# Performance work log

Hardware: AMD Instinct MI355X
Metric: run time of the kernel (lower is better)

Reference implementation:

```python
import jax, jax.numpy as jnp
import numpy as np

NUM_HEADS = 8
# iRPE 'product' piecewise params with ratio=1.9
ALPHA, BETA, GAMMA = 1.9, 3.8, 15.2
BETA_INT = 4                       # round(BETA)
S = 2 * BETA_INT + 1               # 9 buckets per axis
NUM_BUCKETS = S * S                # 81


def _piecewise_index(d):
    # d: float relative coordinate; linear inside |d|<=alpha, log-spaced outside, clipped at beta
    ad = jnp.abs(d)
    log_part = jnp.sign(d) * jnp.round(
        jnp.minimum(ALPHA + jnp.log(jnp.maximum(ad, ALPHA) / ALPHA)
                    / np.log(GAMMA / ALPHA) * (BETA - ALPHA), BETA))
    idx = jnp.where(ad <= ALPHA, jnp.round(d), log_part)
    return jnp.clip(idx, -BETA_INT, BETA_INT).astype(jnp.int32)


def _bucket_ids(side):
    # 2D product bucketing over a side x side grid -> [N, N] int32 bucket ids in [0, 81)
    coords = jnp.stack(jnp.meshgrid(jnp.arange(side), jnp.arange(side), indexing='ij'),
                       axis=-1).reshape(-1, 2).astype(jnp.float32)
    diff = coords[:, None, :] - coords[None, :, :]          # [N, N, 2]
    by = _piecewise_index(diff[..., 0]) + BETA_INT
    bx = _piecewise_index(diff[..., 1]) + BETA_INT
    return by * S + bx


def _layernorm(x, g, b):
    mu = jnp.mean(x, axis=-1, keepdims=True)
    var = jnp.mean(jnp.square(x - mu), axis=-1, keepdims=True)
    return (x - mu) * jax.lax.rsqrt(var + 1e-5) * g + b


def _mlp(x, w1, b1, w2, b2):
    h = jax.nn.gelu(x @ w1 + b1, approximate=False)
    return h @ w2 + b2


def _attention(q, k, v, bucket, tq, tk, tv, wp, bp):
    # q,k,v: [B, N, C]; bucket: [N, N]; tq/tk/tv: [81, hd] (shared across heads)
    B, Nq, C = q.shape
    Nk = k.shape[1]
    hd = C // NUM_HEADS
    scale = hd ** -0.5
    qh = q.reshape(B, Nq, NUM_HEADS, hd).transpose(0, 2, 1, 3)   # [B,H,Nq,hd]
    kh = k.reshape(B, Nk, NUM_HEADS, hd).transpose(0, 2, 1, 3)
    vh = v.reshape(B, Nk, NUM_HEADS, hd).transpose(0, 2, 1, 3)
    attn = jnp.einsum('bhid,bhjd->bhij', qh, kh) * scale          # [B,H,Nq,Nk]
    # rpe_k: contextual bias from q: q . tk[bucket(i,j)]
    lk = jnp.einsum('bhid,cd->bhic', qh, tk)                      # [B,H,Nq,81]
    rows = jnp.arange(Nq)[:, None]
    attn = attn + lk[:, :, rows, bucket]
    # rpe_q: contextual bias from scaled k, then transposed onto (i,j)
    lq = jnp.einsum('bhjd,cd->bhjc', kh * scale, tq)              # [B,H,Nk,81]
    bq = lq[:, :, jnp.arange(Nk)[:, None], bucket]                # [B,H,Nk,Nq] (j,i)
    attn = attn + bq.transpose(0, 1, 3, 2)
    attn = jax.nn.softmax(attn, axis=-1)
    outh = jnp.einsum('bhij,bhjd->bhid', attn, vh)
    # rpe_v: attn-weighted sum of tv[bucket(i,j)]
    outh = outh + jnp.einsum('bhij,ijd->bhid', attn, tv[bucket])
    out = outh.transpose(0, 2, 1, 3).reshape(B, Nq, C)
    return out @ wp + bp


def setup_inputs() -> dict:
    key = jax.random.key(0)
    ks = jax.random.split(key, 16)
    B, N, C, H = 4, 1024, 512, 2048
    w = lambda k, s: (jax.random.normal(k, s, jnp.float32) * 0.02)
    return {
        'x0': jax.random.normal(ks[0], (B, N, C), jnp.float32),
        'x1': jax.random.normal(ks[1], (B, N, C), jnp.float32),
        'ln00_g': jnp.ones((C,), jnp.float32), 'ln00_b': jnp.zeros((C,), jnp.float32),
        'ln01_g': jnp.ones((C,), jnp.float32), 'ln01_b': jnp.zeros((C,), jnp.float32),
        'ln10_g': jnp.ones((C,), jnp.float32), 'ln10_b': jnp.zeros((C,), jnp.float32),
        'ln11_g': jnp.ones((C,), jnp.float32), 'ln11_b': jnp.zeros((C,), jnp.float32),
        'w_qkv0': w(ks[2], (C, 3 * C)), 'b_qkv0': jnp.zeros((3 * C,), jnp.float32),
        'w_qkv1': w(ks[3], (C, 3 * C)), 'b_qkv1': jnp.zeros((3 * C,), jnp.float32),
        'w_proj': w(ks[4], (C, C)), 'b_proj': jnp.zeros((C,), jnp.float32),
        'table_q': w(ks[5], (NUM_BUCKETS, C // NUM_HEADS)),
        'table_k': w(ks[6], (NUM_BUCKETS, C // NUM_HEADS)),
        'table_v': w(ks[7], (NUM_BUCKETS, C // NUM_HEADS)),
        'w_fc1_0': w(ks[8], (C, H)), 'b_fc1_0': jnp.zeros((H,), jnp.float32),
        'w_fc2_0': w(ks[9], (H, C)), 'b_fc2_0': jnp.zeros((C,), jnp.float32),
        'w_fc1_1': w(ks[10], (C, H)), 'b_fc1_1': jnp.zeros((H,), jnp.float32),
        'w_fc2_1': w(ks[11], (H, C)), 'b_fc2_1': jnp.zeros((C,), jnp.float32),
    }


def reference(x0, x1, ln00_g, ln00_b, ln01_g, ln01_b, ln10_g, ln10_b, ln11_g, ln11_b,
              w_qkv0, b_qkv0, w_qkv1, b_qkv1, w_proj, b_proj,
              table_q, table_k, table_v,
              w_fc1_0, b_fc1_0, w_fc2_0, b_fc2_0, w_fc1_1, b_fc1_1, w_fc2_1, b_fc2_1):
    B, N, C = x0.shape
    side = int(np.sqrt(N))
    bucket = _bucket_ids(side)                                   # [N, N]
    qkv0 = _layernorm(x0, ln00_g, ln00_b) @ w_qkv0 + b_qkv0
    q0, k0, v0 = jnp.split(qkv0, 3, axis=-1)
    qkv1 = _layernorm(x1, ln01_g, ln01_b) @ w_qkv1 + b_qkv1
    q1, k1, v1 = jnp.split(qkv1, 3, axis=-1)
    # shared cross-attention module (same proj + rpe tables both directions)
    x0 = x0 + _attention(q0, k1, v1, bucket, table_q, table_k, table_v, w_proj, b_proj)
    x1 = x1 + _attention(q1, k0, v0, bucket, table_q, table_k, table_v, w_proj, b_proj)
    x0 = x0 + _mlp(_layernorm(x0, ln10_g, ln10_b), w_fc1_0, b_fc1_0, w_fc2_0, b_fc2_0)
    x1 = x1 + _mlp(_layernorm(x1, ln11_g, ln11_b), w_fc1_1, b_fc1_1, w_fc2_1, b_fc2_1)
    return (x0, x1)
```

## Files before the change

kernel.cpp:

```cpp
#include <hip/hip_runtime.h>
#include <hip/hip_bf16.h>
#include <math.h>

#define NFULL 1024
#define CDIM  512
#define HD    64
#define NH    8

typedef __attribute__((ext_vector_type(8))) short s16x8;
typedef __attribute__((ext_vector_type(4))) short s16x4;
typedef __attribute__((ext_vector_type(4))) float f32x4;

__device__ __forceinline__ float b2f(unsigned short u) {
  return __uint_as_float((unsigned)u << 16);
}
__device__ __forceinline__ unsigned short f2b(float f) {
  unsigned u = __float_as_uint(f);
  return (unsigned short)((u + 0x7FFFu + ((u >> 16) & 1u)) >> 16);
}

__device__ __forceinline__ int pwidx(int d) {
  int ad = d < 0 ? -d : d;
  if (ad <= 1) return d;
  float v = 1.9f + logf((float)ad * (1.0f / 1.9f)) * (1.9f / 2.0794415416798357f);
  v = fminf(v, 3.8f);
  int m = (int)rintf(v);
  if (m > 4) m = 4;
  return d > 0 ? m : -m;
}

__global__ __launch_bounds__(256) void ln_kernel(const float* __restrict__ x,
                                                 const float* __restrict__ g,
                                                 const float* __restrict__ be,
                                                 __hip_bfloat16* __restrict__ y) {
  __shared__ float red[8];
  int row = blockIdx.x, tid = threadIdx.x;
  const float* xr = x + (size_t)row * CDIM;
  float v0 = xr[tid], v1 = xr[tid + 256];
  float s = v0 + v1;
#pragma unroll
  for (int off = 32; off; off >>= 1) s += __shfl_xor(s, off);
  int wid = tid >> 6, lane = tid & 63;
  if (!lane) red[wid] = s;
  __syncthreads();
  float mu = (red[0] + red[1] + red[2] + red[3]) * (1.0f / 512.0f);
  float d0 = v0 - mu, d1 = v1 - mu;
  float q = d0 * d0 + d1 * d1;
#pragma unroll
  for (int off = 32; off; off >>= 1) q += __shfl_xor(q, off);
  if (!lane) red[4 + wid] = q;
  __syncthreads();
  float var = (red[4] + red[5] + red[6] + red[7]) * (1.0f / 512.0f);
  float rstd = rsqrtf(var + 1e-5f);
  __hip_bfloat16* yr = y + (size_t)row * CDIM;
  yr[tid]       = __float2bfloat16(d0 * rstd * g[tid]       + be[tid]);
  yr[tid + 256] = __float2bfloat16(d1 * rstd * g[tid + 256] + be[tid + 256]);
}

__global__ __launch_bounds__(256) void wtrans_kernel(const float* __restrict__ W,
                                                     __hip_bfloat16* __restrict__ Wt,
                                                     int K, int N) {
  __shared__ float t[32][33];
  int n0 = blockIdx.x * 32, k0 = blockIdx.y * 32;
  int c = threadIdx.x, r0 = threadIdx.y;
#pragma unroll
  for (int rr = 0; rr < 32; rr += 8) t[r0 + rr][c] = W[(size_t)(k0 + r0 + rr) * N + n0 + c];
  __syncthreads();
#pragma unroll
  for (int rr = 0; rr < 32; rr += 8)
    Wt[(size_t)(n0 + r0 + rr) * K + k0 + c] = __float2bfloat16(t[c][r0 + rr]);
}

__device__ __forceinline__ float gelu_f(float x) {
  return 0.5f * x * (1.0f + erff(x * 0.7071067811865475f));
}

template <int ACT, int RES, int OUTBF>
__global__ __launch_bounds__(256, 1) void gemm_bf16(const short* __restrict__ A,
                                                    const short* __restrict__ Bt,
                                                    const float* __restrict__ bias,
                                                    const float* __restrict__ res,
                                                    void* __restrict__ Cout,
                                                    int M, int N, int K) {
  __shared__ __attribute__((aligned(16))) short As[128 * 40];
  __shared__ __attribute__((aligned(16))) short Bs[128 * 40];
  const int tid = threadIdx.x;
  const int bm = blockIdx.y * 128, bn = blockIdx.x * 128;
  const int w = tid >> 6, l = tid & 63;
  const int wr = w >> 1, wc = w & 1;
  const int lr = l & 15, lg = l >> 4;
  const int sr = tid >> 1, sh = (tid & 1) * 16;

  f32x4 acc[4][4] = {};

  for (int k0 = 0; k0 < K; k0 += 32) {
    __syncthreads();
    const float4* ga = (const float4*)(A + (size_t)(bm + sr) * K + k0 + sh);
    const float4* gb = (const float4*)(Bt + (size_t)(bn + sr) * K + k0 + sh);
    float4 a0 = ga[0], a1 = ga[1];
    float4 b0 = gb[0], b1 = gb[1];
    *(float4*)&As[sr * 40 + sh]     = a0;
    *(float4*)&As[sr * 40 + sh + 8] = a1;
    *(float4*)&Bs[sr * 40 + sh]     = b0;
    *(float4*)&Bs[sr * 40 + sh + 8] = b1;
    __syncthreads();
    s16x8 af[4], bf[4];
#pragma unroll
    for (int mi = 0; mi < 4; ++mi)
      af[mi] = *(const s16x8*)&As[(wr * 64 + mi * 16 + lr) * 40 + lg * 8];
#pragma unroll
    for (int ni = 0; ni < 4; ++ni)
      bf[ni] = *(const s16x8*)&Bs[(wc * 64 + ni * 16 + lr) * 40 + lg * 8];
#pragma unroll
    for (int mi = 0; mi < 4; ++mi)
#pragma unroll
      for (int ni = 0; ni < 4; ++ni)
        acc[mi][ni] = __builtin_amdgcn_mfma_f32_16x16x32_bf16(af[mi], bf[ni], acc[mi][ni], 0, 0, 0);
  }
  float bv[4];
#pragma unroll
  for (int ni = 0; ni < 4; ++ni) bv[ni] = bias[bn + wc * 64 + ni * 16 + lr];
#pragma unroll
  for (int mi = 0; mi < 4; ++mi) {
#pragma unroll
    for (int j = 0; j < 4; ++j) {
      int row = bm + wr * 64 + mi * 16 + lg * 4 + j;
#pragma unroll
      for (int ni = 0; ni < 4; ++ni) {
        int col = bn + wc * 64 + ni * 16 + lr;
        float vv = acc[mi][ni][j] + bv[ni];
        if (ACT) vv = gelu_f(vv);
        if (RES) vv += res[(size_t)row * N + col];
        if (OUTBF) ((__hip_bfloat16*)Cout)[(size_t)row * N + col] = __float2bfloat16(vv);
        else       ((float*)Cout)[(size_t)row * N + col] = vv;
      }
    }
  }
}

__global__ __launch_bounds__(256) void prep_kernel(const short* __restrict__ qkvb,
                                                   short* __restrict__ Qb,
                                                   short* __restrict__ Kb,
                                                   short* __restrict__ Vtb) {
  __shared__ short vlds[64 * 72];
  const int tid = threadIdx.x;
  const int n0 = blockIdx.x * 64;
  const int b = blockIdx.y;

#pragma unroll 4
  for (int it = 0; it < 32; ++it) {
    int e = tid + it * 256;
    int n = e >> 7, c8 = (e & 127) * 8;
    s16x8 v = *(const s16x8*)(qkvb + ((size_t)(b * NFULL + n0 + n)) * 1536 + c8);
    int hh = c8 >> 6, d8 = c8 & 63;
    if (hh < 8)
      *(s16x8*)(Qb + ((size_t)(b * 8 + hh) * NFULL + n0 + n) * 64 + d8) = v;
    else
      *(s16x8*)(Kb + ((size_t)(b * 8 + hh - 8) * NFULL + n0 + n) * 64 + d8) = v;
  }
  for (int hh = 0; hh < 8; ++hh) {
    __syncthreads();
#pragma unroll
    for (int rep = 0; rep < 2; ++rep) {
      int n = (tid >> 3) + rep * 32, d8 = (tid & 7) * 8;
      *(s16x8*)&vlds[n * 72 + d8] =
          *(const s16x8*)(qkvb + ((size_t)(b * NFULL + n0 + n)) * 1536 + 1024 + hh * 64 + d8);
    }
    __syncthreads();
#pragma unroll
    for (int rep = 0; rep < 2; ++rep) {
      int d = (tid >> 3) + rep * 32, n8 = (tid & 7) * 8;
      s16x8 o;
#pragma unroll
      for (int u = 0; u < 8; ++u) o[u] = vlds[(n8 + u) * 72 + d];
      *(s16x8*)(Vtb + ((size_t)(b * 8 + hh) * 64 + d) * NFULL + n0 + n8) = o;
    }
  }
}

__global__ __launch_bounds__(256) void bias_gemm(const short* __restrict__ Xb,
                                                 const float* __restrict__ Tg,
                                                 short* __restrict__ outg,
                                                 float scl) {
  __shared__ __attribute__((aligned(16))) short tlds[96 * 88];
  const int tid = threadIdx.x;
  const int w = tid >> 6, l = tid & 63;
  const int g = l >> 4, i15 = l & 15;
  const int tile = blockIdx.x, h = blockIdx.y, b = blockIdx.z;
  const size_t bh = (size_t)(b * NH + h);

  for (int f = tid; f < 81 * 16; f += 256) {
    int c = f >> 4, d4 = (f & 15) * 4;
    float4 t4 = *(const float4*)&Tg[c * 64 + d4];
    s16x4 s4 = {(short)f2b(t4.x), (short)f2b(t4.y), (short)f2b(t4.z), (short)f2b(t4.w)};
    *(s16x4*)&tlds[c * 88 + d4] = s4;
  }
  __syncthreads();

  const int r0w = tile * 128 + w * 32;
  s16x8 af[2][2];
#pragma unroll
  for (int nk = 0; nk < 2; ++nk) {
    const short* xr = Xb + (bh * NFULL + r0w + nk * 16 + i15) * 64 + g * 8;
    af[nk][0] = *(const s16x8*)(xr);
    af[nk][1] = *(const s16x8*)(xr + 32);
  }
#pragma unroll
  for (int c0i = 0; c0i < 6; ++c0i) {
    int c0 = c0i * 16;
    s16x8 bf0 = *(const s16x8*)&tlds[(c0 + i15) * 88 + g * 8];
    s16x8 bf1 = *(const s16x8*)&tlds[(c0 + i15) * 88 + 32 + g * 8];
#pragma unroll
    for (int nk = 0; nk < 2; ++nk) {
      f32x4 acc = {0.f, 0.f, 0.f, 0.f};
      acc = __builtin_amdgcn_mfma_f32_16x16x32_bf16(af[nk][0], bf0, acc, 0, 0, 0);
      acc = __builtin_amdgcn_mfma_f32_16x16x32_bf16(af[nk][1], bf1, acc, 0, 0, 0);
      int c = c0 + i15;
      if (c < 81) {
#pragma unroll
        for (int r = 0; r < 4; ++r) {
          int n = r0w + nk * 16 + g * 4 + r;
          outg[(bh * NFULL + n) * 84 + c] = (short)f2b(acc[r] * scl);
        }
      }
    }
  }
}

__global__ __launch_bounds__(256, 3) void attn_mfma(const short* __restrict__ Qb,
                                                    const short* __restrict__ Kb,
                                                    const short* __restrict__ Vtb,
                                                    const short* __restrict__ lkg,
                                                    const short* __restrict__ lqg,
                                                    const float* __restrict__ tv,
                                                    __hip_bfloat16* __restrict__ o) {
  __shared__ __attribute__((aligned(16))) short pbuf[4][1024];
  __shared__ float wbf[64 * 81];
  __shared__ __attribute__((aligned(16))) float tvf[81 * 64];
  __shared__ short pwy9[63], pwx4[63];

  const int tid = threadIdx.x;
  const int w = tid >> 6, l = tid & 63;
  const int g = l >> 4, i15 = l & 15;
  const int i0 = blockIdx.x * 64;
  const int h = blockIdx.y, b = blockIdx.z;
  const size_t bh = (size_t)(b * NH + h);
  const int i = i0 + w * 16 + i15;

  for (int f = tid; f < 1296; f += 256) ((float4*)tvf)[f] = ((const float4*)tv)[f];
  for (int f = tid; f < 5184; f += 256) wbf[f] = 0.f;
  if (tid < 63) {
    int pv = pwidx(tid - 31);
    pwy9[tid] = (short)((pv + 4) * 9);
    pwx4[tid] = (short)(pv + 4);
  }
  __syncthreads();

  const short* qrow = Qb + (bh * NFULL + i) * 64 + g * 8;
  const s16x8 qf0 = *(const s16x8*)(qrow);
  const s16x8 qf1 = *(const s16x8*)(qrow + 32);
  const unsigned short* lkrow = (const unsigned short*)(lkg + (bh * NFULL + i) * 84);
  const unsigned short* lqb = (const unsigned short*)(lqg + bh * NFULL * 84);
  const short* Kbase = Kb + bh * NFULL * 64;
  const short* Vbase = Vtb + bh * 64 * NFULL;
  const int iy = i >> 5, ix = i & 31;
  char* pwc = (char*)&pbuf[w][0];
  const int swz = (i15 & 7) << 4;
  float* wrow = &wbf[(w * 16 + i15) * 81];

  f32x4 oacc[4] = {};
  float psum = 0.f;

  for (int T = 0; T < 16; ++T) {
    const int j0 = T * 64;
    s16x8 kf[4][2], vf[4][2];
#pragma unroll
    for (int jc = 0; jc < 4; ++jc) {
      const short* kr = Kbase + (size_t)(j0 + jc * 16 + i15) * 64 + g * 8;
      kf[jc][0] = *(const s16x8*)(kr);
      kf[jc][1] = *(const s16x8*)(kr + 32);
    }
#pragma unroll
    for (int nc = 0; nc < 4; ++nc) {
      const short* vr = Vbase + (size_t)(nc * 16 + i15) * NFULL + j0 + g * 8;
      vf[nc][0] = *(const s16x8*)(vr);
      vf[nc][1] = *(const s16x8*)(vr + 32);
    }
    f32x4 sacc[4];
    const f32x4 zz = {0.f, 0.f, 0.f, 0.f};
#pragma unroll
    for (int jc = 0; jc < 4; ++jc) {
      sacc[jc] = __builtin_amdgcn_mfma_f32_16x16x32_bf16(kf[jc][0], qf0, zz, 0, 0, 0);
      sacc[jc] = __builtin_amdgcn_mfma_f32_16x16x32_bf16(kf[jc][1], qf1, sacc[jc], 0, 0, 0);
    }
#pragma unroll
    for (int jc = 0; jc < 4; ++jc) {
      s16x4 pv4;
#pragma unroll
      for (int r = 0; r < 4; ++r) {
        int j = j0 + jc * 16 + g * 4 + r;
        int jy = j >> 5, jx = j & 31;
        int bb = (int)pwy9[iy - jy + 31] + (int)pwx4[ix - jx + 31];
        float sv = sacc[jc][r] * 0.125f + b2f(lkrow[bb]) + b2f(lqb[(size_t)j * 84 + 80 - bb]);
        float p = __expf(sv);
        psum += p;
        atomicAdd(&wrow[bb], p);
        pv4[r] = (short)f2b(p);
      }
      *(s16x4*)(pwc + i15 * 128 + ((jc * 32 + g * 8) ^ swz)) = pv4;
    }
    s16x8 pbf0 = *(const s16x8*)(pwc + i15 * 128 + ((16 * g) ^ swz));
    s16x8 pbf1 = *(const s16x8*)(pwc + i15 * 128 + ((64 + 16 * g) ^ swz));
#pragma unroll
    for (int nc = 0; nc < 4; ++nc) {
      oacc[nc] = __builtin_amdgcn_mfma_f32_16x16x32_bf16(vf[nc][0], pbf0, oacc[nc], 0, 0, 0);
      oacc[nc] = __builtin_amdgcn_mfma_f32_16x16x32_bf16(vf[nc][1], pbf1, oacc[nc], 0, 0, 0);
    }
  }

  psum += __shfl_xor(psum, 16);
  psum += __shfl_xor(psum, 32);
  const float rn = 1.0f / psum;

  float tva[4][4] = {};
  for (int c1 = 0; c1 < 81; ++c1) {
    float wv = wrow[c1];
#pragma unroll
    for (int nc = 0; nc < 4; ++nc) {
      float4 t4 = *(const float4*)&tvf[c1 * 64 + nc * 16 + g * 4];
      tva[nc][0] = fmaf(wv, t4.x, tva[nc][0]);
      tva[nc][1] = fmaf(wv, t4.y, tva[nc][1]);
      tva[nc][2] = fmaf(wv, t4.z, tva[nc][2]);
      tva[nc][3] = fmaf(wv, t4.w, tva[nc][3]);
    }
  }

  short* ob = (short*)o + ((size_t)b * NFULL + i) * CDIM + h * 64;
#pragma unroll
  for (int nc = 0; nc < 4; ++nc) {
    s16x4 o4;
#pragma unroll
    for (int r = 0; r < 4; ++r) o4[r] = (short)f2b((oacc[nc][r] + tva[nc][r]) * rn);
    *(s16x4*)(ob + nc * 16 + g * 4) = o4;
  }
}

extern "C" void kernel_launch(void* const* d_in, const int* in_sizes, int n_in,
                              void* d_out, int out_size, void* d_ws, size_t ws_size,
                              hipStream_t stream) {
  (void)in_sizes; (void)n_in; (void)out_size; (void)ws_size;
  const float* x0 = (const float*)d_in[0];
  const float* x1 = (const float*)d_in[1];
  const float* ln00_g = (const float*)d_in[2];
  const float* ln00_b = (const float*)d_in[3];
  const float* ln01_g = (const float*)d_in[4];
  const float* ln01_b = (const float*)d_in[5];
  const float* ln10_g = (const float*)d_in[6];
  const float* ln10_b = (const float*)d_in[7];
  const float* ln11_g = (const float*)d_in[8];
  const float* ln11_b = (const float*)d_in[9];
  const float* w_qkv0 = (const float*)d_in[10];
  const float* b_qkv0 = (const float*)d_in[11];
  const float* w_qkv1 = (const float*)d_in[12];
  const float* b_qkv1 = (const float*)d_in[13];
  const float* w_proj = (const float*)d_in[14];
  const float* b_proj = (const float*)d_in[15];
  const float* table_q = (const float*)d_in[16];
  const float* table_k = (const float*)d_in[17];
  const float* table_v = (const float*)d_in[18];
  const float* w_fc1_0 = (const float*)d_in[19];
  const float* b_fc1_0 = (const float*)d_in[20];
  const float* w_fc2_0 = (const float*)d_in[21];
  const float* b_fc2_0 = (const float*)d_in[22];
  const float* w_fc1_1 = (const float*)d_in[23];
  const float* b_fc1_1 = (const float*)d_in[24];
  const float* w_fc2_1 = (const float*)d_in[25];
  const float* b_fc2_1 = (const float*)d_in[26];

  char* base = (char*)d_ws;
  short* qkvb0 = (short*)(base + 0);
  short* qkvb1 = (short*)(base + 12582912);
  short* Qb0   = (short*)(base + 25165824);
  short* Kb0   = (short*)(base + 29360128);
  short* Vtb0  = (short*)(base + 33554432);
  short* Qb1   = (short*)(base + 37748736);
  short* Kb1   = (short*)(base + 41943040);
  short* Vtb1  = (short*)(base + 46137344);
  short* lkg   = (short*)(base + 50331648);
  short* lqg   = (short*)(base + 55836672);
  short* obuf  = (short*)(base + 61341696);
  __hip_bfloat16* xnb = (__hip_bfloat16*)(base + 65536000);
  __hip_bfloat16* wq0t  = (__hip_bfloat16*)(base + 69730304);
  __hip_bfloat16* wq1t  = (__hip_bfloat16*)(base + 71303168);
  __hip_bfloat16* wpt   = (__hip_bfloat16*)(base + 72876032);
  __hip_bfloat16* wf10t = (__hip_bfloat16*)(base + 73400320);
  __hip_bfloat16* wf20t = (__hip_bfloat16*)(base + 75497472);
  __hip_bfloat16* wf11t = (__hip_bfloat16*)(base + 77594624);
  __hip_bfloat16* wf21t = (__hip_bfloat16*)(base + 79691776);
  short* hbufb = (short*)(base + 0);
  float* dout0 = (float*)d_out;
  float* dout1 = dout0 + (size_t)4 * 1024 * 512;

  const int M = 4096;

  wtrans_kernel<<<dim3(48, 16), dim3(32, 8), 0, stream>>>(w_qkv0, wq0t, 512, 1536);
  wtrans_kernel<<<dim3(48, 16), dim3(32, 8), 0, stream>>>(w_qkv1, wq1t, 512, 1536);
  wtrans_kernel<<<dim3(16, 16), dim3(32, 8), 0, stream>>>(w_proj, wpt, 512, 512);
  wtrans_kernel<<<dim3(64, 16), dim3(32, 8), 0, stream>>>(w_fc1_0, wf10t, 512, 2048);
  wtrans_kernel<<<dim3(16, 64), dim3(32, 8), 0, stream>>>(w_fc2_0, wf20t, 2048, 512);
  wtrans_kernel<<<dim3(64, 16), dim3(32, 8), 0, stream>>>(w_fc1_1, wf11t, 512, 2048);
  wtrans_kernel<<<dim3(16, 64), dim3(32, 8), 0, stream>>>(w_fc2_1, wf21t, 2048, 512);

  ln_kernel<<<M, 256, 0, stream>>>(x0, ln00_g, ln00_b, xnb);
  gemm_bf16<0, 0, 1><<<dim3(12, 32), 256, 0, stream>>>((const short*)xnb, (const short*)wq0t,
                                                       b_qkv0, nullptr, qkvb0, M, 1536, 512);
  ln_kernel<<<M, 256, 0, stream>>>(x1, ln01_g, ln01_b, xnb);
  gemm_bf16<0, 0, 1><<<dim3(12, 32), 256, 0, stream>>>((const short*)xnb, (const short*)wq1t,
                                                       b_qkv1, nullptr, qkvb1, M, 1536, 512);

  prep_kernel<<<dim3(16, 4), 256, 0, stream>>>(qkvb0, Qb0, Kb0, Vtb0);
  prep_kernel<<<dim3(16, 4), 256, 0, stream>>>(qkvb1, Qb1, Kb1, Vtb1);

  bias_gemm<<<dim3(8, 8, 4), 256, 0, stream>>>(Qb0, table_k, lkg, 1.0f);
  bias_gemm<<<dim3(8, 8, 4), 256, 0, stream>>>(Kb1, table_q, lqg, 0.125f);
  attn_mfma<<<dim3(16, 8, 4), 256, 0, stream>>>(Qb0, Kb1, Vtb1, lkg, lqg, table_v,
                                                (__hip_bfloat16*)obuf);
  gemm_bf16<0, 1, 0><<<dim3(4, 32), 256, 0, stream>>>(obuf, (const short*)wpt,
                                                      b_proj, x0, dout0, M, 512, 512);

  bias_gemm<<<dim3(8, 8, 4), 256, 0, stream>>>(Qb1, table_k, lkg, 1.0f);
  bias_gemm<<<dim3(8, 8, 4), 256, 0, stream>>>(Kb0, table_q, lqg, 0.125f);
  attn_mfma<<<dim3(16, 8, 4), 256, 0, stream>>>(Qb1, Kb0, Vtb0, lkg, lqg, table_v,
                                                (__hip_bfloat16*)obuf);
  gemm_bf16<0, 1, 0><<<dim3(4, 32), 256, 0, stream>>>(obuf, (const short*)wpt,
                                                      b_proj, x1, dout1, M, 512, 512);

  ln_kernel<<<M, 256, 0, stream>>>(dout0, ln10_g, ln10_b, xnb);
  gemm_bf16<1, 0, 1><<<dim3(16, 32), 256, 0, stream>>>((const short*)xnb, (const short*)wf10t,
                                                       b_fc1_0, nullptr, hbufb, M, 2048, 512);
  gemm_bf16<0, 1, 0><<<dim3(4, 32), 256, 0, stream>>>(hbufb, (const short*)wf20t,
                                                      b_fc2_0, dout0, dout0, M, 512, 2048);

  ln_kernel<<<M, 256, 0, stream>>>(dout1, ln11_g, ln11_b, xnb);
  gemm_bf16<1, 0, 1><<<dim3(16, 32), 256, 0, stream>>>((const short*)xnb, (const short*)wf11t,
                                                       b_fc1_1, nullptr, hbufb, M, 2048, 512);
  gemm_bf16<0, 1, 0><<<dim3(4, 32), 256, 0, stream>>>(hbufb, (const short*)wf21t,
                                                      b_fc2_1, dout1, dout1, M, 512, 2048);
}
```

Before: 864.5 us.

## Double-buffer K/V register loads and stage lk rows in LDS in attention kernel

```diff
diff --git a/kernel.cpp b/kernel.cpp
--- a/kernel.cpp
+++ b/kernel.cpp
@@ -227,6 +227,72 @@
   }
 }
 
+#define ATTN_STEP(J0, J0N, KF, VF, KFN, VFN, BY0, BY1, BY0N, BY1N)                       \
+  {                                                                                      \
+                              \
+    unsigned short lqv[4][4];                                                            \
+    _Pragma("unroll") for (int jc = 0; jc < 4; ++jc) {                                   \
+      _Pragma("unroll") for (int r = 0; r < 4; ++r) {                                    \
+        int bb = ((jc & 2) ? (BY1) : (BY0)) + bx8[jc & 1][r];                            \
+        lqv[jc][r] = lqb[(size_t)((J0) + jc * 16 + g * 4 + r) * 84 + 80 - bb];           \
+      }                                                                                  \
+    }                                                                                    \
+                                                    \
+    f32x4 sacc[4];                                                                       \
+    _Pragma("unroll") for (int jc = 0; jc < 4; ++jc) {                                   \
+      f32x4 zz = {0.f, 0.f, 0.f, 0.f};                                                   \
+      sacc[jc] = __builtin_amdgcn_mfma_f32_16x16x32_bf16(KF[jc][0], qf0, zz, 0, 0, 0);   \
+      sacc[jc] = __builtin_amdgcn_mfma_f32_16x16x32_bf16(KF[jc][1], qf1, sacc[jc], 0, 0, 0); \
+    }                                                                                    \
+                          \
+    {                                                                                    \
+      int j0w = (J0N) & 1023;                                                            \
+      _Pragma("unroll") for (int jc = 0; jc < 4; ++jc) {                                 \
+        const short* kr = Kb_h + (size_t)(j0w + jc * 16 + i15) * 64 + g * 8;             \
+        KFN[jc][0] = *(const s16x8*)(kr);                                                \
+        KFN[jc][1] = *(const s16x8*)(kr + 32);                                           \
+      }                                                                                  \
+      _Pragma("unroll") for (int nc = 0; nc < 4; ++nc) {                                 \
+        const short* vr = Vb_h + (size_t)(nc * 16 + i15) * NFULL + j0w + g * 8;          \
+        VFN[nc][0] = *(const s16x8*)(vr);                                                \
+        VFN[nc][1] = *(const s16x8*)(vr + 32);                                           \
+      }                                                                                  \
+      int jy0n = j0w >> 5;                                                               \
+      BY0N = (int)pwy9s[iy - jy0n + 31];                                                 \
+      BY1N = (int)pwy9s[iy - jy0n + 30];                                                 \
+    }                                                                                    \
+                                                             \
+    s16x4 pvall[4];                                                                      \
+    _Pragma("unroll") for (int jc = 0; jc < 4; ++jc) {                                   \
+      s16x4 pv4;                                                                         \
+      _Pragma("unroll") for (int r = 0; r < 4; ++r) {                                    \
+        int bb = ((jc & 2) ? (BY1) : (BY0)) + bx8[jc & 1][r];                            \
+        float sv = sacc[jc][r] * 0.125f + b2f(lkw[bb]) + b2f(lqv[jc][r]);                \
+        float p = __expf(sv);                                                            \
+        psum += p;                                                                       \
+        pv4[r] = (short)f2b(p);                                                          \
+      }                                                                                  \
+      pvall[jc] = pv4;                                                                   \
+      *(s16x4*)(pwc + i15 * 128 + ((jc * 32 + g * 8) ^ swz)) = pv4;                      \
+    }                                                                                    \
+                                                                         \
+    {                                                                                    \
+      s16x8 pbf0 = *(const s16x8*)(pwc + i15 * 128 + ((16 * g) ^ swz));                  \
+      s16x8 pbf1 = *(const s16x8*)(pwc + i15 * 128 + ((64 + 16 * g) ^ swz));             \
+      _Pragma("unroll") for (int nc = 0; nc < 4; ++nc) {                                 \
+        oacc[nc] = __builtin_amdgcn_mfma_f32_16x16x32_bf16(VF[nc][0], pbf0, oacc[nc], 0, 0, 0); \
+        oacc[nc] = __builtin_amdgcn_mfma_f32_16x16x32_bf16(VF[nc][1], pbf1, oacc[nc], 0, 0, 0); \
+      }                                                                                  \
+    }                                                                                    \
+                           \
+    _Pragma("unroll") for (int jc = 0; jc < 4; ++jc) {                                   \
+      _Pragma("unroll") for (int r = 0; r < 4; ++r) {                                    \
+        int bb = ((jc & 2) ? (BY1) : (BY0)) + bx8[jc & 1][r];                            \
+        atomicAdd(&wbf[rowi * 81 + bb], b2f((unsigned short)pvall[jc][r]));              \
+      }                                                                                  \
+    }                                                                                    \
+  }
+
 __global__ __launch_bounds__(256, 3) void attn_mfma(const short* __restrict__ Qb,
                                                     const short* __restrict__ Kb,
                                                     const short* __restrict__ Vtb,
@@ -234,88 +300,75 @@
                                                     const short* __restrict__ lqg,
                                                     const float* __restrict__ tv,
                                                     __hip_bfloat16* __restrict__ o) {
+  __shared__ __attribute__((aligned(16))) short lkb[64 * 84];
   __shared__ __attribute__((aligned(16))) short pbuf[4][1024];
   __shared__ float wbf[64 * 81];
-  __shared__ __attribute__((aligned(16))) float tvf[81 * 64];
-  __shared__ short pwy9[63], pwx4[63];
+  __shared__ short pwy9s[64], pwx4s[64];
 
   const int tid = threadIdx.x;
   const int w = tid >> 6, l = tid & 63;
   const int g = l >> 4, i15 = l & 15;
-  const int i0 = blockIdx.x * 64;
-  const int h = blockIdx.y, b = blockIdx.z;
+  const int f = blockIdx.x + 16 * (blockIdx.y + 8 * blockIdx.z);
+  const int hb = f & 31, tile = f >> 5;
+  const int b = hb >> 3, h = hb & 7;
+  const int i0 = tile * 64;
   const size_t bh = (size_t)(b * NH + h);
   const int i = i0 + w * 16 + i15;
-
-  for (int f = tid; f < 1296; f += 256) ((float4*)tvf)[f] = ((const float4*)tv)[f];
-  for (int f = tid; f < 5184; f += 256) wbf[f] = 0.f;
-  if (tid < 63) {
-    int pv = pwidx(tid - 31);
-    pwy9[tid] = (short)((pv + 4) * 9);
-    pwx4[tid] = (short)(pv + 4);
+  const int rowi = w * 16 + i15;
+
+  {
+    const s16x4* lksrc = (const s16x4*)(lkg + (bh * NFULL + i0) * 84);
+    for (int ff = tid; ff < 1344; ff += 256) ((s16x4*)lkb)[ff] = lksrc[ff];
+    for (int ff = tid; ff < 5184; ff += 256) wbf[ff] = 0.f;
+    if (tid < 63) {
+      int pv = pwidx(tid - 31);
+      pwy9s[tid] = (short)((pv + 4) * 9);
+      pwx4s[tid] = (short)(pv + 4);
+    }
   }
   __syncthreads();
 
   const short* qrow = Qb + (bh * NFULL + i) * 64 + g * 8;
   const s16x8 qf0 = *(const s16x8*)(qrow);
   const s16x8 qf1 = *(const s16x8*)(qrow + 32);
-  const unsigned short* lkrow = (const unsigned short*)(lkg + (bh * NFULL + i) * 84);
+  const short* Kb_h = Kb + bh * NFULL * 64;
+  const short* Vb_h = Vtb + bh * 64 * NFULL;
   const unsigned short* lqb = (const unsigned short*)(lqg + bh * NFULL * 84);
-  const short* Kbase = Kb + bh * NFULL * 64;
-  const short* Vbase = Vtb + bh * 64 * NFULL;
+  const unsigned short* lkw = (const unsigned short*)lkb + rowi * 84;
   const int iy = i >> 5, ix = i & 31;
   char* pwc = (char*)&pbuf[w][0];
   const int swz = (i15 & 7) << 4;
-  float* wrow = &wbf[(w * 16 + i15) * 81];
+
+  int bx8[2][4];
+#pragma unroll
+  for (int hi = 0; hi < 2; ++hi)
+#pragma unroll
+    for (int r = 0; r < 4; ++r) bx8[hi][r] = (int)pwx4s[ix - (hi * 16 + g * 4 + r) + 31];
 
   f32x4 oacc[4] = {};
   float psum = 0.f;
 
-  for (int T = 0; T < 16; ++T) {
-    const int j0 = T * 64;
-    s16x8 kf[4][2], vf[4][2];
-#pragma unroll
-    for (int jc = 0; jc < 4; ++jc) {
-      const short* kr = Kbase + (size_t)(j0 + jc * 16 + i15) * 64 + g * 8;
-      kf[jc][0] = *(const s16x8*)(kr);
-      kf[jc][1] = *(const s16x8*)(kr + 32);
-    }
-#pragma unroll
-    for (int nc = 0; nc < 4; ++nc) {
-      const short* vr = Vbase + (size_t)(nc * 16 + i15) * NFULL + j0 + g * 8;
-      vf[nc][0] = *(const s16x8*)(vr);
-      vf[nc][1] = *(const s16x8*)(vr + 32);
-    }
-    f32x4 sacc[4];
-    const f32x4 zz = {0.f, 0.f, 0.f, 0.f};
-#pragma unroll
-    for (int jc = 0; jc < 4; ++jc) {
-      sacc[jc] = __builtin_amdgcn_mfma_f32_16x16x32_bf16(kf[jc][0], qf0, zz, 0, 0, 0);
-      sacc[jc] = __builtin_amdgcn_mfma_f32_16x16x32_bf16(kf[jc][1], qf1, sacc[jc], 0, 0, 0);
-    }
-#pragma unroll
-    for (int jc = 0; jc < 4; ++jc) {
-      s16x4 pv4;
-#pragma unroll
-      for (int r = 0; r < 4; ++r) {
-        int j = j0 + jc * 16 + g * 4 + r;
-        int jy = j >> 5, jx = j & 31;
-        int bb = (int)pwy9[iy - jy + 31] + (int)pwx4[ix - jx + 31];
-        float sv = sacc[jc][r] * 0.125f + b2f(lkrow[bb]) + b2f(lqb[(size_t)j * 84 + 80 - bb]);
-        float p = __expf(sv);
-        psum += p;
-        atomicAdd(&wrow[bb], p);
-        pv4[r] = (short)f2b(p);
-      }
-      *(s16x4*)(pwc + i15 * 128 + ((jc * 32 + g * 8) ^ swz)) = pv4;
-    }
-    s16x8 pbf0 = *(const s16x8*)(pwc + i15 * 128 + ((16 * g) ^ swz));
-    s16x8 pbf1 = *(const s16x8*)(pwc + i15 * 128 + ((64 + 16 * g) ^ swz));
-#pragma unroll
-    for (int nc = 0; nc < 4; ++nc) {
-      oacc[nc] = __builtin_amdgcn_mfma_f32_16x16x32_bf16(vf[nc][0], pbf0, oacc[nc], 0, 0, 0);
-      oacc[nc] = __builtin_amdgcn_mfma_f32_16x16x32_bf16(vf[nc][1], pbf1, oacc[nc], 0, 0, 0);
-    }
+  s16x8 kfA[4][2], vfA[4][2], kfB[4][2], vfB[4][2];
+  int by0A, by1A, by0B, by1B;
+#pragma unroll
+  for (int jc = 0; jc < 4; ++jc) {
+    const short* kr = Kb_h + (size_t)(jc * 16 + i15) * 64 + g * 8;
+    kfA[jc][0] = *(const s16x8*)(kr);
+    kfA[jc][1] = *(const s16x8*)(kr + 32);
+  }
+#pragma unroll
+  for (int nc = 0; nc < 4; ++nc) {
+    const short* vr = Vb_h + (size_t)(nc * 16 + i15) * NFULL + g * 8;
+    vfA[nc][0] = *(const s16x8*)(vr);
+    vfA[nc][1] = *(const s16x8*)(vr + 32);
+  }
+  by0A = (int)pwy9s[iy + 31];
+  by1A = (int)pwy9s[iy + 30];
+
+  for (int t2 = 0; t2 < 8; ++t2) {
+    const int j0 = t2 * 128;
+    ATTN_STEP(j0, j0 + 64, kfA, vfA, kfB, vfB, by0A, by1A, by0B, by1B)
+    ATTN_STEP(j0 + 64, j0 + 128, kfB, vfB, kfA, vfA, by0B, by1B, by0A, by1A)
   }
 
   psum += __shfl_xor(psum, 16);
@@ -324,10 +377,10 @@
 
   float tva[4][4] = {};
   for (int c1 = 0; c1 < 81; ++c1) {
-    float wv = wrow[c1];
+    float wv = wbf[rowi * 81 + c1];
 #pragma unroll
     for (int nc = 0; nc < 4; ++nc) {
-      float4 t4 = *(const float4*)&tvf[c1 * 64 + nc * 16 + g * 4];
+      float4 t4 = *(const float4*)(tv + c1 * 64 + nc * 16 + g * 4);
       tva[nc][0] = fmaf(wv, t4.x, tva[nc][0]);
       tva[nc][1] = fmaf(wv, t4.y, tva[nc][1]);
       tva[nc][2] = fmaf(wv, t4.z, tva[nc][2]);
```

Result: slower. 895.4 us (+3.6%).

## Split attention keys across waves with 16-query tiles and LDS reduction

Applied to the files above, without the earlier changes.

```diff
diff --git a/kernel.cpp b/kernel.cpp
--- a/kernel.cpp
+++ b/kernel.cpp
@@ -227,121 +227,183 @@
   }
 }
 
-__global__ __launch_bounds__(256, 3) void attn_mfma(const short* __restrict__ Qb,
+__global__ __launch_bounds__(256, 2) void attn_mfma(const short* __restrict__ Qb,
                                                     const short* __restrict__ Kb,
                                                     const short* __restrict__ Vtb,
                                                     const short* __restrict__ lkg,
                                                     const short* __restrict__ lqg,
                                                     const float* __restrict__ tv,
                                                     __hip_bfloat16* __restrict__ o) {
+  __shared__ __attribute__((aligned(16))) short lkb[16 * 84];
   __shared__ __attribute__((aligned(16))) short pbuf[4][1024];
-  __shared__ float wbf[64 * 81];
-  __shared__ __attribute__((aligned(16))) float tvf[81 * 64];
-  __shared__ short pwy9[63], pwx4[63];
+  __shared__ float wbf[4][16 * 81];
+  __shared__ float obuf[1024];
+  __shared__ float psums[4][16];
+  __shared__ short pwy9s[64], pwx4s[64];
 
   const int tid = threadIdx.x;
   const int w = tid >> 6, l = tid & 63;
   const int g = l >> 4, i15 = l & 15;
-  const int i0 = blockIdx.x * 64;
-  const int h = blockIdx.y, b = blockIdx.z;
+  const int f = blockIdx.x + 64 * blockIdx.y + 512 * blockIdx.z;
+  const int h = f & 7, tile = (f >> 3) & 63, b = f >> 9;
+  const int i0 = tile * 16;
   const size_t bh = (size_t)(b * NH + h);
-  const int i = i0 + w * 16 + i15;
-
-  for (int f = tid; f < 1296; f += 256) ((float4*)tvf)[f] = ((const float4*)tv)[f];
-  for (int f = tid; f < 5184; f += 256) wbf[f] = 0.f;
-  if (tid < 63) {
-    int pv = pwidx(tid - 31);
-    pwy9[tid] = (short)((pv + 4) * 9);
-    pwx4[tid] = (short)(pv + 4);
+  const int i = i0 + i15;
+
+  {
+    const s16x4* lksrc = (const s16x4*)(lkg + (bh * NFULL + i0) * 84);
+    for (int ff = tid; ff < 336; ff += 256) ((s16x4*)lkb)[ff] = lksrc[ff];
+    float* wflat = &wbf[0][0];
+    for (int ff = tid; ff < 5184; ff += 256) wflat[ff] = 0.f;
+    for (int ff = tid; ff < 1024; ff += 256) obuf[ff] = 0.f;
+    if (tid < 63) {
+      int pv = pwidx(tid - 31);
+      pwy9s[tid] = (short)((pv + 4) * 9);
+      pwx4s[tid] = (short)(pv + 4);
+    }
   }
   __syncthreads();
 
   const short* qrow = Qb + (bh * NFULL + i) * 64 + g * 8;
   const s16x8 qf0 = *(const s16x8*)(qrow);
   const s16x8 qf1 = *(const s16x8*)(qrow + 32);
-  const unsigned short* lkrow = (const unsigned short*)(lkg + (bh * NFULL + i) * 84);
+  const short* Kb_h = Kb + bh * NFULL * 64;
+  const short* Vb_h = Vtb + bh * 64 * NFULL;
   const unsigned short* lqb = (const unsigned short*)(lqg + bh * NFULL * 84);
-  const short* Kbase = Kb + bh * NFULL * 64;
-  const short* Vbase = Vtb + bh * 64 * NFULL;
+  const unsigned short* lkw = (const unsigned short*)lkb + i15 * 84;
   const int iy = i >> 5, ix = i & 31;
   char* pwc = (char*)&pbuf[w][0];
   const int swz = (i15 & 7) << 4;
-  float* wrow = &wbf[(w * 16 + i15) * 81];
+  float* wrow = &wbf[w][i15 * 81];
+
+  int bx8[2][4];
+#pragma unroll
+  for (int hi = 0; hi < 2; ++hi)
+#pragma unroll
+    for (int r = 0; r < 4; ++r) bx8[hi][r] = (int)pwx4s[ix - (hi * 16 + g * 4 + r) + 31];
 
   f32x4 oacc[4] = {};
   float psum = 0.f;
 
-  for (int T = 0; T < 16; ++T) {
-    const int j0 = T * 64;
-    s16x8 kf[4][2], vf[4][2];
+#pragma unroll
+  for (int T = 0; T < 4; ++T) {
+    const int j0 = w * 256 + T * 64;
+    const int jy0 = (j0 >> 5);
+    const int by0 = (int)pwy9s[iy - jy0 + 31];
+    const int by1 = (int)pwy9s[iy - jy0 + 30];
+
+    s16x8 kf[4][2];
 #pragma unroll
     for (int jc = 0; jc < 4; ++jc) {
-      const short* kr = Kbase + (size_t)(j0 + jc * 16 + i15) * 64 + g * 8;
+      const short* kr = Kb_h + (size_t)(j0 + jc * 16 + i15) * 64 + g * 8;
       kf[jc][0] = *(const s16x8*)(kr);
       kf[jc][1] = *(const s16x8*)(kr + 32);
     }
+    unsigned short lqv[4][4];
+#pragma unroll
+    for (int jc = 0; jc < 4; ++jc)
+#pragma unroll
+      for (int r = 0; r < 4; ++r) {
+        int bb = ((jc & 2) ? by1 : by0) + bx8[jc & 1][r];
+        lqv[jc][r] = lqb[(size_t)(j0 + jc * 16 + g * 4 + r) * 84 + 80 - bb];
+      }
+    f32x4 sacc[4];
+#pragma unroll
+    for (int jc = 0; jc < 4; ++jc) {
+      f32x4 zz = {0.f, 0.f, 0.f, 0.f};
+      sacc[jc] = __builtin_amdgcn_mfma_f32_16x16x32_bf16(kf[jc][0], qf0, zz, 0, 0, 0);
+      sacc[jc] = __builtin_amdgcn_mfma_f32_16x16x32_bf16(kf[jc][1], qf1, sacc[jc], 0, 0, 0);
+    }
+    s16x4 pvall[4];
+#pragma unroll
+    for (int jc = 0; jc < 4; ++jc) {
+      s16x4 pv4;
+#pragma unroll
+      for (int r = 0; r < 4; ++r) {
+        int bb = ((jc & 2) ? by1 : by0) + bx8[jc & 1][r];
+        float sv = sacc[jc][r] * 0.125f + b2f(lkw[bb]) + b2f(lqv[jc][r]);
+        float p = __expf(sv);
+        psum += p;
+        pv4[r] = (short)f2b(p);
+      }
+      pvall[jc] = pv4;
+      *(s16x4*)(pwc + i15 * 128 + ((jc * 32 + g * 8) ^ swz)) = pv4;
+    }
+    s16x8 vf[4][2];
 #pragma unroll
     for (int nc = 0; nc < 4; ++nc) {
-      const short* vr = Vbase + (size_t)(nc * 16 + i15) * NFULL + j0 + g * 8;
+      const short* vr = Vb_h + (size_t)(nc * 16 + i15) * NFULL + j0 + g * 8;
       vf[nc][0] = *(const s16x8*)(vr);
       vf[nc][1] = *(const s16x8*)(vr + 32);
     }
-    f32x4 sacc[4];
-    const f32x4 zz = {0.f, 0.f, 0.f, 0.f};
-#pragma unroll
-    for (int jc = 0; jc < 4; ++jc) {
-      sacc[jc] = __builtin_amdgcn_mfma_f32_16x16x32_bf16(kf[jc][0], qf0, zz, 0, 0, 0);
-      sacc[jc] = __builtin_amdgcn_mfma_f32_16x16x32_bf16(kf[jc][1], qf1, sacc[jc], 0, 0, 0);
-    }
-#pragma unroll
-    for (int jc = 0; jc < 4; ++jc) {
-      s16x4 pv4;
+    {
+      s16x8 pbf0 = *(const s16x8*)(pwc + i15 * 128 + ((16 * g) ^ swz));
+      s16x8 pbf1 = *(const s16x8*)(pwc + i15 * 128 + ((64 + 16 * g) ^ swz));
+#pragma unroll
+      for (int nc = 0; nc < 4; ++nc) {
+        oacc[nc] = __builtin_amdgcn_mfma_f32_16x16x32_bf16(vf[nc][0], pbf0, oacc[nc], 0, 0, 0);
+        oacc[nc] = __builtin_amdgcn_mfma_f32_16x16x32_bf16(vf[nc][1], pbf1, oacc[nc], 0, 0, 0);
+      }
+    }
+#pragma unroll
+    for (int jc = 0; jc < 4; ++jc)
 #pragma unroll
       for (int r = 0; r < 4; ++r) {
-        int j = j0 + jc * 16 + g * 4 + r;
-        int jy = j >> 5, jx = j & 31;
-        int bb = (int)pwy9[iy - jy + 31] + (int)pwx4[ix - jx + 31];
-        float sv = sacc[jc][r] * 0.125f + b2f(lkrow[bb]) + b2f(lqb[(size_t)j * 84 + 80 - bb]);
-        float p = __expf(sv);
-        psum += p;
-        atomicAdd(&wrow[bb], p);
-        pv4[r] = (short)f2b(p);
-      }
-      *(s16x4*)(pwc + i15 * 128 + ((jc * 32 + g * 8) ^ swz)) = pv4;
-    }
-    s16x8 pbf0 = *(const s16x8*)(pwc + i15 * 128 + ((16 * g) ^ swz));
-    s16x8 pbf1 = *(const s16x8*)(pwc + i15 * 128 + ((64 + 16 * g) ^ swz));
-#pragma unroll
-    for (int nc = 0; nc < 4; ++nc) {
-      oacc[nc] = __builtin_amdgcn_mfma_f32_16x16x32_bf16(vf[nc][0], pbf0, oacc[nc], 0, 0, 0);
-      oacc[nc] = __builtin_amdgcn_mfma_f32_16x16x32_bf16(vf[nc][1], pbf1, oacc[nc], 0, 0, 0);
-    }
+        int bb = ((jc & 2) ? by1 : by0) + bx8[jc & 1][r];
+        atomicAdd(&wrow[bb], b2f((unsigned short)pvall[jc][r]));
+      }
   }
 
   psum += __shfl_xor(psum, 16);
   psum += __shfl_xor(psum, 32);
-  const float rn = 1.0f / psum;
-
-  float tva[4][4] = {};
-  for (int c1 = 0; c1 < 81; ++c1) {
-    float wv = wrow[c1];
+  if (g == 0) psums[w][i15] = psum;
+#pragma unroll
+  for (int nc = 0; nc < 4; ++nc)
+#pragma unroll
+    for (int r = 0; r < 4; ++r)
+      atomicAdd(&obuf[(nc * 16 + g * 4 + r) * 16 + i15], oacc[nc][r]);
+  __syncthreads();
+
+  {
+    float* w0 = &wbf[0][0];
+    for (int ff = tid; ff < 1296; ff += 256)
+      w0[ff] += wbf[1][ff] + wbf[2][ff] + wbf[3][ff];
+  }
+  __syncthreads();
+
+  {
+    float tva[4][4] = {};
+    for (int c1 = w; c1 < 81; c1 += 4) {
+      float wv = wbf[0][i15 * 81 + c1];
+#pragma unroll
+      for (int nc = 0; nc < 4; ++nc) {
+        float4 t4 = *(const float4*)(tv + c1 * 64 + nc * 16 + g * 4);
+        tva[nc][0] = fmaf(wv, t4.x, tva[nc][0]);
+        tva[nc][1] = fmaf(wv, t4.y, tva[nc][1]);
+        tva[nc][2] = fmaf(wv, t4.z, tva[nc][2]);
+        tva[nc][3] = fmaf(wv, t4.w, tva[nc][3]);
+      }
+    }
+#pragma unroll
+    for (int nc = 0; nc < 4; ++nc)
+#pragma unroll
+      for (int r = 0; r < 4; ++r)
+        atomicAdd(&obuf[(nc * 16 + g * 4 + r) * 16 + i15], tva[nc][r]);
+  }
+  __syncthreads();
+
+  if (w == 0) {
+    float tot = psums[0][i15] + psums[1][i15] + psums[2][i15] + psums[3][i15];
+    float rn = 1.0f / tot;
+    short* ob = (short*)o + ((size_t)b * NFULL + i) * CDIM + h * 64;
 #pragma unroll
     for (int nc = 0; nc < 4; ++nc) {
-      float4 t4 = *(const float4*)&tvf[c1 * 64 + nc * 16 + g * 4];
-      tva[nc][0] = fmaf(wv, t4.x, tva[nc][0]);
-      tva[nc][1] = fmaf(wv, t4.y, tva[nc][1]);
-      tva[nc][2] = fmaf(wv, t4.z, tva[nc][2]);
-      tva[nc][3] = fmaf(wv, t4.w, tva[nc][3]);
-    }
-  }
-
-  short* ob = (short*)o + ((size_t)b * NFULL + i) * CDIM + h * 64;
-#pragma unroll
-  for (int nc = 0; nc < 4; ++nc) {
-    s16x4 o4;
-#pragma unroll
-    for (int r = 0; r < 4; ++r) o4[r] = (short)f2b((oacc[nc][r] + tva[nc][r]) * rn);
-    *(s16x4*)(ob + nc * 16 + g * 4) = o4;
+      s16x4 o4;
+#pragma unroll
+      for (int r = 0; r < 4; ++r)
+        o4[r] = (short)f2b(obuf[(nc * 16 + g * 4 + r) * 16 + i15] * rn);
+      *(s16x4*)(ob + nc * 16 + g * 4) = o4;
+    }
   }
 }
 
@@ -423,14 +485,14 @@
 
   bias_gemm<<<dim3(8, 8, 4), 256, 0, stream>>>(Qb0, table_k, lkg, 1.0f);
   bias_gemm<<<dim3(8, 8, 4), 256, 0, stream>>>(Kb1, table_q, lqg, 0.125f);
-  attn_mfma<<<dim3(16, 8, 4), 256, 0, stream>>>(Qb0, Kb1, Vtb1, lkg, lqg, table_v,
+  attn_mfma<<<dim3(64, 8, 4), 256, 0, stream>>>(Qb0, Kb1, Vtb1, lkg, lqg, table_v,
                                                 (__hip_bfloat16*)obuf);
   gemm_bf16<0, 1, 0><<<dim3(4, 32), 256, 0, stream>>>(obuf, (const short*)wpt,
                                                       b_proj, x0, dout0, M, 512, 512);
 
   bias_gemm<<<dim3(8, 8, 4), 256, 0, stream>>>(Qb1, table_k, lkg, 1.0f);
   bias_gemm<<<dim3(8, 8, 4), 256, 0, stream>>>(Kb0, table_q, lqg, 0.125f);
-  attn_mfma<<<dim3(16, 8, 4), 256, 0, stream>>>(Qb1, Kb0, Vtb0, lkg, lqg, table_v,
+  attn_mfma<<<dim3(64, 8, 4), 256, 0, stream>>>(Qb1, Kb0, Vtb0, lkg, lqg, table_v,
                                                 (__hip_bfloat16*)obuf);
   gemm_bf16<0, 1, 0><<<dim3(4, 32), 256, 0, stream>>>(obuf, (const short*)wpt,
                                                       b_proj, x1, dout1, M, 512, 512);
```

After: 1.017 ms. +17.6%, slower.
